# Kernel optimization log

Measured on AMD Instinct MI355X. Metric: run time of the kernel, lower is better.

## Reference

```python
import jax, jax.numpy as jnp
import numpy as np

N_NODES = 100000
N_EDGES = 1600000
IN_DIM, HID_DIM, OUT_DIM = 128, 64, 64


def setup_inputs() -> dict:
    key = jax.random.key(0)
    ks = jax.random.split(key, 6)
    feat = jax.random.normal(ks[0], (N_NODES, IN_DIM), dtype=jnp.float32)
    W1 = jax.random.normal(ks[1], (IN_DIM, HID_DIM), dtype=jnp.float32) * (IN_DIM ** -0.5)
    W2 = jax.random.normal(ks[2], (HID_DIM, HID_DIM), dtype=jnp.float32) * (HID_DIM ** -0.5)
    W3 = jax.random.normal(ks[3], (HID_DIM, OUT_DIM), dtype=jnp.float32) * (HID_DIM ** -0.5)
    b1 = jnp.zeros((HID_DIM,), jnp.float32)
    b2 = jnp.zeros((HID_DIM,), jnp.float32)
    b3 = jnp.zeros((OUT_DIM,), jnp.float32)
    src = jax.random.randint(ks[4], (N_EDGES,), 0, N_NODES, dtype=jnp.int32)
    dst = jax.random.randint(ks[5], (N_EDGES,), 0, N_NODES, dtype=jnp.int32)
    return {"feat": feat, "W1": W1, "b1": b1, "W2": W2, "b2": b2,
            "W3": W3, "b3": b3, "src": src, "dst": dst}


def _degree_norms(src, dst, n_nodes):
    ones = jnp.ones(src.shape[0], jnp.float32)
    out_deg = jax.ops.segment_sum(ones, src, num_segments=n_nodes)
    in_deg = jax.ops.segment_sum(ones, dst, num_segments=n_nodes)
    # DGL GraphConv norm='both': D_out^{-1/2} on source side, D_in^{-1/2} on dest side
    norm_src = jnp.clip(out_deg, 1.0, None) ** -0.5
    norm_dst = jnp.clip(in_deg, 1.0, None) ** -0.5
    return norm_src, norm_dst


def _graph_conv(h, W, b, src, dst, norm_src, norm_dst, n_nodes):
    # mult-first (in_dim >= out_dim path of DGL; linear so mathematically equivalent)
    hw = (h * norm_src[:, None]) @ W          # [N, out]
    msgs = hw[src]                             # [E, out] gather
    agg = jax.ops.segment_sum(msgs, dst, num_segments=n_nodes)  # [N, out] scatter-add
    return agg * norm_dst[:, None] + b


def reference(feat, W1, b1, W2, b2, W3, b3, src, dst):
    n_nodes = feat.shape[0]
    norm_src, norm_dst = _degree_norms(src, dst, n_nodes)
    h = feat
    for W, b in ((W1, b1), (W2, b2), (W3, b3)):
        h = _graph_conv(h, W, b, src, dst, norm_src, norm_dst, n_nodes)
        h = jax.nn.relu(h)
    return h
```

## Files before the change

kernel.cpp:

```cpp
#include <hip/hip_runtime.h>
#include <hip/hip_fp16.h>
#include <type_traits>

#define N_NODES 100000
#define N_EDGES 1600000
#define CHUNKS 128
#define EPB (N_EDGES / CHUNKS)
#define HALF_NODES 50000
#define WORDS_HALF 12500
#define WORDS_ALL 25000
#define VEC_HALF 3125
#define NBB 98

__global__ void __launch_bounds__(256) hist_kernel(const int* __restrict__ src,
                                                   const int* __restrict__ dst,
                                                   unsigned* __restrict__ histA,
                                                   unsigned* __restrict__ histB) {
    __shared__ __align__(16) unsigned h[WORDS_HALF];
    const int b   = blockIdx.x;
    const int dir = b >> 8;
    const int r   = (b >> 7) & 1;
    const int c   = b & 127;
    const int* __restrict__ ids = dir ? dst : src;
    unsigned* __restrict__ hist = dir ? histB : histA;
    for (int i = threadIdx.x; i < VEC_HALF; i += 256)
        ((uint4*)h)[i] = make_uint4(0u, 0u, 0u, 0u);
    __syncthreads();
    const int base = c * EPB;
    const int lo   = r * HALF_NODES;
    for (int e = base + threadIdx.x; e < base + EPB; e += 256) {
        int id = ids[e] - lo;
        if ((unsigned)id < (unsigned)HALF_NODES)
            atomicAdd(&h[id >> 2], 1u << ((id & 3) * 8));
    }
    __syncthreads();
    unsigned* __restrict__ outp = hist + c * WORDS_ALL + r * WORDS_HALF;
    for (int i = threadIdx.x; i < VEC_HALF; i += 256)
        ((uint4*)outp)[i] = ((const uint4*)h)[i];
}

__global__ void __launch_bounds__(256) degrees_kernel(const unsigned* __restrict__ histA,
                                                      unsigned* __restrict__ histB,
                                                      float* __restrict__ norm_src,
                                                      unsigned* __restrict__ ideg,
                                                      float* __restrict__ norm_dst,
                                                      int* __restrict__ blocksum) {
    __shared__ int sred[256];
    const int t = threadIdx.x;
    const int w = blockIdx.x * 256 + t;
    if (blockIdx.y == 0) {
        if (w >= WORDS_ALL) return;
        unsigned s0 = 0, s1 = 0, s2 = 0, s3 = 0;
#pragma unroll 4
        for (int c = 0; c < CHUNKS; ++c) {
            unsigned v = histA[c * WORDS_ALL + w];
            s0 += v & 255u; s1 += (v >> 8) & 255u; s2 += (v >> 16) & 255u; s3 += v >> 24;
        }
        const int n = w * 4;
        norm_src[n + 0] = rsqrtf((float)(s0 > 1u ? s0 : 1u));
        norm_src[n + 1] = rsqrtf((float)(s1 > 1u ? s1 : 1u));
        norm_src[n + 2] = rsqrtf((float)(s2 > 1u ? s2 : 1u));
        norm_src[n + 3] = rsqrtf((float)(s3 > 1u ? s3 : 1u));
    } else {
        unsigned s0 = 0, s1 = 0, s2 = 0, s3 = 0;
        if (w < WORDS_ALL) {
            unsigned run = 0;
#pragma unroll 4
            for (int c = 0; c < CHUNKS; ++c) {
                unsigned v = histB[c * WORDS_ALL + w];
                histB[c * WORDS_ALL + w] = run;
                run += v;
            }
            s0 = run & 255u; s1 = (run >> 8) & 255u; s2 = (run >> 16) & 255u; s3 = run >> 24;
            const int n = w * 4;
            ideg[n + 0] = s0; ideg[n + 1] = s1; ideg[n + 2] = s2; ideg[n + 3] = s3;
            norm_dst[n + 0] = rsqrtf((float)(s0 > 1u ? s0 : 1u));
            norm_dst[n + 1] = rsqrtf((float)(s1 > 1u ? s1 : 1u));
            norm_dst[n + 2] = rsqrtf((float)(s2 > 1u ? s2 : 1u));
            norm_dst[n + 3] = rsqrtf((float)(s3 > 1u ? s3 : 1u));
        }
        sred[t] = (int)(s0 + s1 + s2 + s3);
        __syncthreads();
        for (int off = 128; off > 0; off >>= 1) {
            if (t < off) sred[t] += sred[t + off];
            __syncthreads();
        }
        if (t == 0) blocksum[blockIdx.x] = sred[0];
    }
}

__global__ void scan_sums_kernel(const int* __restrict__ blocksum, int* __restrict__ blockoff,
                                 int* __restrict__ row_start) {
    __shared__ int s[128];
    const int t = threadIdx.x;
    int v0 = (t < NBB) ? blocksum[t] : 0;
    s[t] = v0;
    __syncthreads();
    for (int off = 1; off < 128; off <<= 1) {
        int v = (t >= off) ? s[t - off] : 0;
        __syncthreads();
        s[t] += v;
        __syncthreads();
    }
    if (t < NBB) blockoff[t] = s[t] - v0;
    if (t == 0) row_start[N_NODES] = N_EDGES;
}

__global__ void __launch_bounds__(256) write_offsets_kernel(const unsigned* __restrict__ ideg,
                                                            const int* __restrict__ blockoff,
                                                            int* __restrict__ row_start) {
    __shared__ int s[256];
    const int t = threadIdx.x;
    const int w = blockIdx.x * 256 + t;
    unsigned c0 = 0, c1 = 0, c2 = 0, c3 = 0;
    if (w < WORDS_ALL) {
        uint4 v = *(const uint4*)&ideg[w * 4];
        c0 = v.x; c1 = v.y; c2 = v.z; c3 = v.w;
    }
    int tot = (int)(c0 + c1 + c2 + c3);
    s[t] = tot;
    __syncthreads();
    for (int off = 1; off < 256; off <<= 1) {
        int v = (t >= off) ? s[t - off] : 0;
        __syncthreads();
        s[t] += v;
        __syncthreads();
    }
    if (w < WORDS_ALL) {
        int e = blockoff[blockIdx.x] + s[t] - tot;
        int4 o;
        o.x = e;
        o.y = e + (int)c0;
        o.z = e + (int)(c0 + c1);
        o.w = e + (int)(c0 + c1 + c2);
        *(int4*)&row_start[w * 4] = o;
    }
}

__global__ void __launch_bounds__(256) scatter_kernel(const int* __restrict__ src,
                                                      const int* __restrict__ dst,
                                                      const unsigned* __restrict__ histB,
                                                      const int* __restrict__ row_start,
                                                      int* __restrict__ sorted_src) {
    __shared__ __align__(16) unsigned cur[WORDS_HALF];
    const int c = blockIdx.x;
    const int r = blockIdx.y;
    const unsigned* __restrict__ pref = histB + c * WORDS_ALL + r * WORDS_HALF;
    for (int i = threadIdx.x; i < VEC_HALF; i += 256)
        ((uint4*)cur)[i] = ((const uint4*)pref)[i];
    __syncthreads();
    const int base = c * EPB;
    const int lo   = r * HALF_NODES;
    for (int e = base + threadIdx.x; e < base + EPB; e += 256) {
        int d  = dst[e];
        int dl = d - lo;
        if ((unsigned)dl < (unsigned)HALF_NODES) {
            unsigned old = atomicAdd(&cur[dl >> 2], 1u << ((dl & 3) * 8));
            unsigned rk  = (old >> ((dl & 3) * 8)) & 255u;
            sorted_src[row_start[d] + (int)rk] = src[e];
        }
    }
}

template <int K, typename IN>
__global__ void __launch_bounds__(256) gemm_kernel(const IN* __restrict__ h,
                                                   const float* __restrict__ W,
                                                   const float* __restrict__ norm_src,
                                                   __half* __restrict__ out) {
    __shared__ float Ws[K * 64];
    __shared__ float hs[64][68];
    const int t  = threadIdx.x;
    const int ty = t >> 4;
    const int tx = t & 15;
    const int nb = blockIdx.x * 64;

#pragma unroll
    for (int i = 0; i < K * 16 / 256; ++i)
        ((float4*)Ws)[i * 256 + t] = ((const float4*)W)[i * 256 + t];

    float a[4][4];
#pragma unroll
    for (int m = 0; m < 4; ++m)
#pragma unroll
        for (int j = 0; j < 4; ++j) a[m][j] = 0.f;

    for (int kk = 0; kk < K; kk += 64) {
        __syncthreads();
        if constexpr (std::is_same<IN, float>::value) {
#pragma unroll
            for (int r = 0; r < 4; ++r) {
                int e = r * 1024 + t * 4;
                int m = e >> 6, k = e & 63;
                int node = nb + m;
                float4 v = make_float4(0.f, 0.f, 0.f, 0.f);
                if (node < N_NODES) v = *(const float4*)&h[(size_t)node * K + kk + k];
                *(float4*)&hs[m][k] = v;
            }
        } else {
#pragma unroll
            for (int r = 0; r < 2; ++r) {
                int e = r * 2048 + t * 8;
                int m = e >> 6, k = e & 63;
                int node = nb + m;
                float4 lo = make_float4(0.f, 0.f, 0.f, 0.f);
                float4 hi = make_float4(0.f, 0.f, 0.f, 0.f);
                if (node < N_NODES) {
                    uint4 raw = *reinterpret_cast<const uint4*>(&h[(size_t)node * K + kk + k]);
                    float2 f0 = __half22float2(*reinterpret_cast<__half2*>(&raw.x));
                    float2 f1 = __half22float2(*reinterpret_cast<__half2*>(&raw.y));
                    float2 f2 = __half22float2(*reinterpret_cast<__half2*>(&raw.z));
                    float2 f3 = __half22float2(*reinterpret_cast<__half2*>(&raw.w));
                    lo = make_float4(f0.x, f0.y, f1.x, f1.y);
                    hi = make_float4(f2.x, f2.y, f3.x, f3.y);
                }
                *(float4*)&hs[m][k]     = lo;
                *(float4*)&hs[m][k + 4] = hi;
            }
        }
        __syncthreads();

#pragma unroll 4
        for (int k = 0; k < 64; k += 4) {
            float w[4][4], hr[4][4];
#pragma unroll
            for (int i = 0; i < 4; ++i) {
                float4 wv = *(const float4*)&Ws[(kk + k + i) * 64 + tx * 4];
                w[i][0] = wv.x; w[i][1] = wv.y; w[i][2] = wv.z; w[i][3] = wv.w;
            }
#pragma unroll
            for (int m = 0; m < 4; ++m) {
                float4 hv = *(const float4*)&hs[ty * 4 + m][k];
                hr[m][0] = hv.x; hr[m][1] = hv.y; hr[m][2] = hv.z; hr[m][3] = hv.w;
            }
#pragma unroll
            for (int m = 0; m < 4; ++m)
#pragma unroll
                for (int i = 0; i < 4; ++i)
#pragma unroll
                    for (int j = 0; j < 4; ++j)
                        a[m][j] = fmaf(hr[m][i], w[i][j], a[m][j]);
        }
    }

#pragma unroll
    for (int m = 0; m < 4; ++m) {
        int node = nb + ty * 4 + m;
        if (node < N_NODES) {
            float ns = norm_src[node];
            __half2 p0 = __floats2half2_rn(a[m][0] * ns, a[m][1] * ns);
            __half2 p1 = __floats2half2_rn(a[m][2] * ns, a[m][3] * ns);
            uint2 raw;
            raw.x = *reinterpret_cast<unsigned*>(&p0);
            raw.y = *reinterpret_cast<unsigned*>(&p1);
            *reinterpret_cast<uint2*>(&out[(size_t)node * 64 + tx * 4]) = raw;
        }
    }
}

template <typename OUT>
__global__ void __launch_bounds__(256) agg_kernel(const __half* __restrict__ hw,
                                                  const int* __restrict__ sorted_src,
                                                  const int* __restrict__ row_start,
                                                  const float* __restrict__ norm_dst,
                                                  const float* __restrict__ b,
                                                  OUT* __restrict__ out) {
    const int node = blockIdx.x * 8 + (threadIdx.x >> 5);
    const int l32  = threadIdx.x & 31;
    const int g    = l32 >> 3;
    const int q    = l32 & 7;
    const int beg = row_start[node];
    const int end = row_start[node + 1];

    float a[8];
#pragma unroll
    for (int j = 0; j < 8; ++j) a[j] = 0.f;

#define GCN_GATHER(idx)                                                                       \
    do {                                                                                      \
        uint4 raw = *reinterpret_cast<const uint4*>(&hw[(size_t)sorted_src[idx] * 64 + q * 8]); \
        float2 f0 = __half22float2(*reinterpret_cast<__half2*>(&raw.x));                      \
        float2 f1 = __half22float2(*reinterpret_cast<__half2*>(&raw.y));                      \
        float2 f2 = __half22float2(*reinterpret_cast<__half2*>(&raw.z));                      \
        float2 f3 = __half22float2(*reinterpret_cast<__half2*>(&raw.w));                      \
        a[0] += f0.x; a[1] += f0.y; a[2] += f1.x; a[3] += f1.y;                               \
        a[4] += f2.x; a[5] += f2.y; a[6] += f3.x; a[7] += f3.y;                               \
    } while (0)

    for (int e = beg + g; e < end; e += 16) {
        int i1 = e + 4, i2 = e + 8, i3 = e + 12;
        GCN_GATHER(e);
        if (i1 < end) GCN_GATHER(i1);
        if (i2 < end) GCN_GATHER(i2);
        if (i3 < end) GCN_GATHER(i3);
    }
#undef GCN_GATHER

#pragma unroll
    for (int j = 0; j < 8; ++j) {
        a[j] += __shfl_xor(a[j], 8);
        a[j] += __shfl_xor(a[j], 16);
    }

    if (g == 0) {
        float ns = norm_dst[node];
        float o[8];
#pragma unroll
        for (int j = 0; j < 8; ++j) {
            float v = fmaf(a[j], ns, b[q * 8 + j]);
            o[j] = v > 0.f ? v : 0.f;
        }
        if constexpr (std::is_same<OUT, float>::value) {
            *(float4*)&out[(size_t)node * 64 + q * 8]     = make_float4(o[0], o[1], o[2], o[3]);
            *(float4*)&out[(size_t)node * 64 + q * 8 + 4] = make_float4(o[4], o[5], o[6], o[7]);
        } else {
            __half2 p0 = __floats2half2_rn(o[0], o[1]);
            __half2 p1 = __floats2half2_rn(o[2], o[3]);
            __half2 p2 = __floats2half2_rn(o[4], o[5]);
            __half2 p3 = __floats2half2_rn(o[6], o[7]);
            uint4 raw;
            raw.x = *reinterpret_cast<unsigned*>(&p0);
            raw.y = *reinterpret_cast<unsigned*>(&p1);
            raw.z = *reinterpret_cast<unsigned*>(&p2);
            raw.w = *reinterpret_cast<unsigned*>(&p3);
            *reinterpret_cast<uint4*>(&out[(size_t)node * 64 + q * 8]) = raw;
        }
    }
}

extern "C" void kernel_launch(void* const* d_in, const int* in_sizes, int n_in,
                              void* d_out, int out_size, void* d_ws, size_t ws_size,
                              hipStream_t stream) {
    const float* feat = (const float*)d_in[0];
    const float* W1   = (const float*)d_in[1];
    const float* b1   = (const float*)d_in[2];
    const float* W2   = (const float*)d_in[3];
    const float* b2   = (const float*)d_in[4];
    const float* W3   = (const float*)d_in[5];
    const float* b3   = (const float*)d_in[6];
    const int*   src  = (const int*)d_in[7];
    const int*   dst  = (const int*)d_in[8];
    float* out = (float*)d_out;

    char* ws = (char*)d_ws;
    size_t off = 0;
    auto alloc = [&](size_t bytes) { char* p = ws + off; off += (bytes + 255) & ~size_t(255); return p; };
    float*    norm_src   = (float*)alloc(N_NODES * 4);
    float*    norm_dst   = (float*)alloc(N_NODES * 4);
    unsigned* ideg       = (unsigned*)alloc(N_NODES * 4);
    int*      row_start  = (int*)alloc((N_NODES + 1) * 4);
    int*      blocksum   = (int*)alloc(NBB * 4);
    int*      blockoff   = (int*)alloc(NBB * 4);
    int*      sorted_src = (int*)alloc(N_EDGES * 4);
    __half*   hw         = (__half*)alloc(N_NODES * 64 * 2);
    __half*   hb         = (__half*)alloc(N_NODES * 64 * 2);

    unsigned* histA = (unsigned*)hw;
    unsigned* histB = (unsigned*)hb;

    hist_kernel<<<512, 256, 0, stream>>>(src, dst, histA, histB);
    degrees_kernel<<<dim3(NBB, 2), 256, 0, stream>>>(histA, histB, norm_src, ideg, norm_dst, blocksum);

    scan_sums_kernel<<<1, 128, 0, stream>>>(blocksum, blockoff, row_start);
    write_offsets_kernel<<<NBB, 256, 0, stream>>>(ideg, blockoff, row_start);

    scatter_kernel<<<dim3(128, 2), 256, 0, stream>>>(src, dst, histB, row_start, sorted_src);

    const int GEMM_GRID = (N_NODES + 63) / 64;
    const int AGG_GRID  = N_NODES / 8;

    gemm_kernel<128, float><<<GEMM_GRID, 256, 0, stream>>>(feat, W1, norm_src, hw);
    agg_kernel<__half><<<AGG_GRID, 256, 0, stream>>>(hw, sorted_src, row_start, norm_dst, b1, hb);

    gemm_kernel<64, __half><<<GEMM_GRID, 256, 0, stream>>>(hb, W2, norm_src, hw);
    agg_kernel<__half><<<AGG_GRID, 256, 0, stream>>>(hw, sorted_src, row_start, norm_dst, b2, hb);

    gemm_kernel<64, __half><<<GEMM_GRID, 256, 0, stream>>>(hb, W3, norm_src, hw);
    agg_kernel<float><<<AGG_GRID, 256, 0, stream>>>(hw, sorted_src, row_start, norm_dst, b3, out);
}
```

Before: 355.8 us.

## Use MFMA f16 matrix instructions for the node feature GEMM

Replaces the LDS-tiled scalar FMA GEMM with MFMA 16x16x32 f16 instructions. Weights are converted to f16 and stored in LDS in fragment layout, and each wave loads its A fragments directly from global memory. This cuts ALU work and LDS traffic in the GEMM stage. In exchange the fp32 input features are rounded to f16 before the multiply, and the outputs are written as scalar half stores.

```diff
diff --git a/kernel.cpp b/kernel.cpp
--- a/kernel.cpp
+++ b/kernel.cpp
@@ -11,6 +11,9 @@
 #define WORDS_ALL 25000
 #define VEC_HALF 3125
 #define NBB 98
+
+typedef _Float16 half8 __attribute__((ext_vector_type(8)));
+typedef float f32x4 __attribute__((ext_vector_type(4)));
 
 __global__ void __launch_bounds__(256) hist_kernel(const int* __restrict__ src,
                                                    const int* __restrict__ dst,
@@ -167,92 +170,70 @@
                                                    const float* __restrict__ W,
                                                    const float* __restrict__ norm_src,
                                                    __half* __restrict__ out) {
-    __shared__ float Ws[K * 64];
-    __shared__ float hs[64][68];
-    const int t  = threadIdx.x;
-    const int ty = t >> 4;
-    const int tx = t & 15;
-    const int nb = blockIdx.x * 64;
-
-#pragma unroll
-    for (int i = 0; i < K * 16 / 256; ++i)
-        ((float4*)Ws)[i * 256 + t] = ((const float4*)W)[i * 256 + t];
-
-    float a[4][4];
-#pragma unroll
-    for (int m = 0; m < 4; ++m)
-#pragma unroll
-        for (int j = 0; j < 4; ++j) a[m][j] = 0.f;
-
-    for (int kk = 0; kk < K; kk += 64) {
-        __syncthreads();
-        if constexpr (std::is_same<IN, float>::value) {
-#pragma unroll
-            for (int r = 0; r < 4; ++r) {
-                int e = r * 1024 + t * 4;
-                int m = e >> 6, k = e & 63;
-                int node = nb + m;
-                float4 v = make_float4(0.f, 0.f, 0.f, 0.f);
-                if (node < N_NODES) v = *(const float4*)&h[(size_t)node * K + kk + k];
-                *(float4*)&hs[m][k] = v;
+    constexpr int KSTEPS = K / 32;
+    __shared__ __align__(16) _Float16 Wlds[KSTEPS * 4 * 64 * 8];
+    const int t = threadIdx.x;
+
+    for (int f = t; f < KSTEPS * 4 * 64; f += 256) {
+        int l  = f & 63;
+        int c  = (f >> 6) & 3;
+        int ks = f >> 8;
+        int kbase = ks * 32 + (l >> 4) * 8;
+        int col   = c * 16 + (l & 15);
+        half8 frag;
+#pragma unroll
+        for (int i = 0; i < 8; ++i)
+            frag[i] = (_Float16)W[(kbase + i) * 64 + col];
+        *(half8*)&Wlds[(size_t)f * 8] = frag;
+    }
+    __syncthreads();
+
+    const int w    = t >> 6;
+    const int l    = t & 63;
+    const int arow = blockIdx.x * 64 + w * 16 + (l & 15);
+    const int koff = (l >> 4) * 8;
+    const bool arow_ok = arow < N_NODES;
+
+    f32x4 acc[4];
+#pragma unroll
+    for (int c = 0; c < 4; ++c) acc[c] = (f32x4)(0.f);
+
+#pragma unroll
+    for (int ks = 0; ks < KSTEPS; ++ks) {
+        half8 a;
+        if (arow_ok) {
+            if constexpr (std::is_same<IN, float>::value) {
+                const float* p = &h[(size_t)arow * K + ks * 32 + koff];
+                float4 lo = *(const float4*)p;
+                float4 hi = *(const float4*)(p + 4);
+                a[0] = (_Float16)lo.x; a[1] = (_Float16)lo.y;
+                a[2] = (_Float16)lo.z; a[3] = (_Float16)lo.w;
+                a[4] = (_Float16)hi.x; a[5] = (_Float16)hi.y;
+                a[6] = (_Float16)hi.z; a[7] = (_Float16)hi.w;
+            } else {
+                a = *(const half8*)((const void*)&h[(size_t)arow * K + ks * 32 + koff]);
             }
         } else {
 #pragma unroll
-            for (int r = 0; r < 2; ++r) {
-                int e = r * 2048 + t * 8;
-                int m = e >> 6, k = e & 63;
-                int node = nb + m;
-                float4 lo = make_float4(0.f, 0.f, 0.f, 0.f);
-                float4 hi = make_float4(0.f, 0.f, 0.f, 0.f);
-                if (node < N_NODES) {
-                    uint4 raw = *reinterpret_cast<const uint4*>(&h[(size_t)node * K + kk + k]);
-                    float2 f0 = __half22float2(*reinterpret_cast<__half2*>(&raw.x));
-                    float2 f1 = __half22float2(*reinterpret_cast<__half2*>(&raw.y));
-                    float2 f2 = __half22float2(*reinterpret_cast<__half2*>(&raw.z));
-                    float2 f3 = __half22float2(*reinterpret_cast<__half2*>(&raw.w));
-                    lo = make_float4(f0.x, f0.y, f1.x, f1.y);
-                    hi = make_float4(f2.x, f2.y, f3.x, f3.y);
-                }
-                *(float4*)&hs[m][k]     = lo;
-                *(float4*)&hs[m][k + 4] = hi;
+            for (int i = 0; i < 8; ++i) a[i] = (_Float16)0.f;
+        }
+#pragma unroll
+        for (int c = 0; c < 4; ++c) {
+            half8 b = *(const half8*)&Wlds[(size_t)((ks * 4 + c) * 64 + l) * 8];
+            acc[c] = __builtin_amdgcn_mfma_f32_16x16x32_f16(a, b, acc[c], 0, 0, 0);
+        }
+    }
+
+    const int drow0 = blockIdx.x * 64 + w * 16 + (l >> 4) * 4;
+#pragma unroll
+    for (int r = 0; r < 4; ++r) {
+        int row = drow0 + r;
+        if (row < N_NODES) {
+            float ns = norm_src[row];
+#pragma unroll
+            for (int c = 0; c < 4; ++c) {
+                out[(size_t)row * 64 + c * 16 + (l & 15)] = __float2half(acc[c][r] * ns);
             }
-        }
-        __syncthreads();
-
-#pragma unroll 4
-        for (int k = 0; k < 64; k += 4) {
-            float w[4][4], hr[4][4];
-#pragma unroll
-            for (int i = 0; i < 4; ++i) {
-                float4 wv = *(const float4*)&Ws[(kk + k + i) * 64 + tx * 4];
-                w[i][0] = wv.x; w[i][1] = wv.y; w[i][2] = wv.z; w[i][3] = wv.w;
-            }
-#pragma unroll
-            for (int m = 0; m < 4; ++m) {
-                float4 hv = *(const float4*)&hs[ty * 4 + m][k];
-                hr[m][0] = hv.x; hr[m][1] = hv.y; hr[m][2] = hv.z; hr[m][3] = hv.w;
-            }
-#pragma unroll
-            for (int m = 0; m < 4; ++m)
-#pragma unroll
-                for (int i = 0; i < 4; ++i)
-#pragma unroll
-                    for (int j = 0; j < 4; ++j)
-                        a[m][j] = fmaf(hr[m][i], w[i][j], a[m][j]);
-        }
-    }
-
-#pragma unroll
-    for (int m = 0; m < 4; ++m) {
-        int node = nb + ty * 4 + m;
-        if (node < N_NODES) {
-            float ns = norm_src[node];
-            __half2 p0 = __floats2half2_rn(a[m][0] * ns, a[m][1] * ns);
-            __half2 p1 = __floats2half2_rn(a[m][2] * ns, a[m][3] * ns);
-            uint2 raw;
-            raw.x = *reinterpret_cast<unsigned*>(&p0);
-            raw.y = *reinterpret_cast<unsigned*>(&p1);
-            *reinterpret_cast<uint2*>(&out[(size_t)node * 64 + tx * 4]) = raw;
         }
     }
 }
```

Result: faster. 326.9 us (-8.1%).
